# Kernel tuning notes

Measured on AMD Instinct MI355X. Metric: run time of the kernel, lower is better.

Reference implementation:

```python
import jax, jax.numpy as jnp
import numpy as np

H, W = 1280, 1920          # dense depth canvas (hardcoded in the torch module)
OUT_H, OUT_W = 427, 640    # kornia resize target
BIG = 1e9                  # sentinel coordinate for 'no seed yet'
FX = FY = 1000.0
CX, CY = 960.0, 640.0


def _jfa_nearest(valid):
    """1+JFA jump-flooding: (H,W) bool -> (H,W,2) float coords of nearest valid pixel.
    Replaces the faiss GpuIndexFlatL2 exact 1-NN over pixel coordinates."""
    rr, cc = jnp.meshgrid(jnp.arange(H, dtype=jnp.float32),
                          jnp.arange(W, dtype=jnp.float32), indexing='ij')
    coords = jnp.stack([rr, cc], axis=-1)                      # (H,W,2)
    nearest = jnp.where(valid[..., None], coords, BIG)
    best = jnp.sum((coords - nearest) ** 2, axis=-1)           # squared dist to current seed
    row_idx = jnp.arange(H)[:, None]
    col_idx = jnp.arange(W)[None, :]
    steps = [1, 1024, 512, 256, 128, 64, 32, 16, 8, 4, 2, 1]   # 1+JFA schedule, max dim 1920
    for k in steps:
        for dy in (-k, 0, k):
            for dx in (-k, 0, k):
                if dy == 0 and dx == 0:
                    continue
                cand = jnp.roll(nearest, (dy, dx), axis=(0, 1))
                src_r = row_idx - dy
                src_c = col_idx - dx
                ok = (src_r >= 0) & (src_r < H) & (src_c >= 0) & (src_c < W)
                cand = jnp.where(ok[..., None], cand, BIG)
                d = jnp.sum((coords - cand) ** 2, axis=-1)
                better = d < best
                best = jnp.where(better, d, best)
                nearest = jnp.where(better[..., None], cand, nearest)
    return nearest


def _one(points, pose, extrinsic, intrinsic):
    # projection path uses points.detach() in the torch code -> stop_gradient here
    p = jax.lax.stop_gradient(points)
    pts_world = p @ pose[:3, :3].T + pose[:3, 3]
    cam = pts_world @ extrinsic[:3, :3].T + extrinsic[:3, 3]
    proj = cam @ intrinsic.T
    u = proj[:, 0] / proj[:, 2]
    v = proj[:, 1] / proj[:, 2]
    r = jnp.floor(v).astype(jnp.int32)   # indices[..., [1,0]] swap -> row = v
    c = jnp.floor(u).astype(jnp.int32)
    depth_vals = jnp.linalg.norm(points, axis=-1)   # differentiable wrt points
    mask = (r >= 0) & (r < H) & (c >= 0) & (c < W)
    rs = jnp.where(mask, r, 0)
    cs = jnp.where(mask, c, 0)
    vals = jnp.where(mask, depth_vals, 0.0)
    # sparse scatter -> dense (duplicates sum, like torch.sparse to_dense)
    depth = jnp.zeros((H, W), jnp.float32).at[rs, cs].add(vals)
    valid = depth != 0
    nearest = jax.lax.stop_gradient(_jfa_nearest(valid))   # integer NN indices: non-diff
    nr = jnp.clip(nearest[..., 0], 0, H - 1).astype(jnp.int32)
    nc = jnp.clip(nearest[..., 1], 0, W - 1).astype(jnp.int32)
    rrf = jnp.arange(H, dtype=jnp.float32)[:, None]
    ccf = jnp.arange(W, dtype=jnp.float32)[None, :]
    dist = jnp.sqrt((rrf - nr.astype(jnp.float32)) ** 2 + (ccf - nc.astype(jnp.float32)) ** 2)
    dist = jnp.where(valid, 0.0, dist)          # dist_matrix only written at invalid pixels
    filled = jnp.where(valid, depth, depth[nr, nc])  # depth*(1-mask) + interpolated*mask
    out = jnp.stack([filled, dist], axis=0)     # (2, H, W)
    return jax.image.resize(out, (2, OUT_H, OUT_W), method='linear')


_batched = jax.jit(jax.vmap(_one))


def setup_inputs() -> dict:
    key = jax.random.key(0)
    B, N = 2, 120000
    ku, kv, kd = jax.random.split(key, 3)
    # sample pixels + depths, back-project so points land on the canvas
    u = jax.random.uniform(ku, (B, N), minval=0.0, maxval=W - 1.0)
    v = jax.random.uniform(kv, (B, N), minval=0.0, maxval=H - 1.0)
    d = jax.random.uniform(kd, (B, N), minval=2.0, maxval=50.0)
    x = (u - CX) * d / FX
    y = (v - CY) * d / FY
    points = jnp.stack([x, y, d], axis=-1).astype(jnp.float32)
    eye4 = jnp.broadcast_to(jnp.eye(4, dtype=jnp.float32), (B, 4, 4))
    K = jnp.array([[FX, 0.0, CX], [0.0, FY, CY], [0.0, 0.0, 1.0]], jnp.float32)
    intrinsic = jnp.broadcast_to(K, (B, 3, 3))
    return {"points": points, "pose": eye4, "extrinsic": eye4, "intrinsic": intrinsic}


def reference(points, pose, extrinsic, intrinsic):
    return _batched(points, pose, extrinsic, intrinsic)   # (B, 2, 427, 640)
```

## Files before the change

### kernel.cpp

```cpp
#include <hip/hip_runtime.h>
#include <math.h>
#include <limits.h>

#define HH 1280
#define WW 1920
#define OUT_H 427
#define OUT_W 640
#define SENT 0x7fff7fff

typedef short short2v __attribute__((ext_vector_type(2)));

__device__ __forceinline__ int dot22(int a, int P) {
#if __has_builtin(__builtin_amdgcn_sdot2)
    short2v s = __builtin_bit_cast(short2v, a) - __builtin_bit_cast(short2v, P);
    return __builtin_amdgcn_sdot2(s, s, 0, false);
#else
    int dr = (a >> 16) - (P >> 16);
    int dc = (short)a - (short)P;
    return dr * dr + dc * dc;
#endif
}
#define PICK(P, cur, dcur, cand)                    \
    {                                               \
        int _d = dot22((cand), (P));                \
        if (_d < (dcur)) { (cur) = (cand); (dcur) = _d; } \
    }

__global__ void scatter_k(const float* __restrict__ pts,
                          const float* __restrict__ pose,
                          const float* __restrict__ extr,
                          const float* __restrict__ intr,
                          float* __restrict__ depth, int N) {
    #pragma clang fp contract(off)
    int t = blockIdx.x * blockDim.x + threadIdx.x;
    int b = blockIdx.y;
    if (t >= N) return;
    const float* p = pts + ((long)b * N + t) * 3;
    float x = p[0], y = p[1], z = p[2];
    const float* P = pose + b * 16;
    const float* E = extr + b * 16;
    const float* K = intr + b * 9;
    float wx = ((x*P[0] + y*P[1]) + z*P[2]) + P[3];
    float wy = ((x*P[4] + y*P[5]) + z*P[6]) + P[7];
    float wz = ((x*P[8] + y*P[9]) + z*P[10]) + P[11];
    float cx = ((wx*E[0] + wy*E[1]) + wz*E[2]) + E[3];
    float cy = ((wx*E[4] + wy*E[5]) + wz*E[6]) + E[7];
    float cz = ((wx*E[8] + wy*E[9]) + wz*E[10]) + E[11];
    float px = (cx*K[0] + cy*K[1]) + cz*K[2];
    float py = (cx*K[3] + cy*K[4]) + cz*K[5];
    float pz = (cx*K[6] + cy*K[7]) + cz*K[8];
    float u = px / pz, v = py / pz;
    int r = (int)floorf(v), c = (int)floorf(u);
    if (r >= 0 && r < HH && c >= 0 && c < WW) {
        float dv = sqrtf((x*x + y*y) + z*z);
        atomicAdd(depth + ((long)b * HH + r) * WW + c, dv);
    }
}


template <bool FIRST>
__global__ __launch_bounds__(512)
void jfa12_k(const void* __restrict__ inv_, int* __restrict__ out, int k) {
    __shared__ int rows[4][WW];
    __shared__ int g1row[WW];
    int i = blockIdx.x, b = blockIdx.y;
    if (FIRST) {
        const float* dep = (const float*)inv_ + (long)b * HH * WW;
        #pragma unroll
        for (int t = 0; t < 4; ++t) {
            int r = i + t * k;
            if (r < HH) {
                const float4* src = reinterpret_cast<const float4*>(dep + (long)r * WW);
                for (int c4 = threadIdx.x; c4 < WW / 4; c4 += 512) {
                    float4 d = src[c4];
                    int4 v;
                    int c0 = c4 * 4, pb = r << 16;
                    v.x = (d.x != 0.0f) ? (pb | c0)       : SENT;
                    v.y = (d.y != 0.0f) ? (pb | (c0 + 1)) : SENT;
                    v.z = (d.z != 0.0f) ? (pb | (c0 + 2)) : SENT;
                    v.w = (d.w != 0.0f) ? (pb | (c0 + 3)) : SENT;
                    reinterpret_cast<int4*>(rows[t])[c4] = v;
                }
            } else {
                int4 sv; sv.x = sv.y = sv.z = sv.w = SENT;
                for (int c4 = threadIdx.x; c4 < WW / 4; c4 += 512)
                    reinterpret_cast<int4*>(rows[t])[c4] = sv;
            }
        }
    } else {
        const int* im = (const int*)inv_ + (long)b * HH * WW;
        #pragma unroll
        for (int t = 0; t < 4; ++t) {
            int r = i + t * k;
            if (r < HH) {
                const int4* src = reinterpret_cast<const int4*>(im + (long)r * WW);
                for (int c4 = threadIdx.x; c4 < WW / 4; c4 += 512)
                    reinterpret_cast<int4*>(rows[t])[c4] = src[c4];
            } else {
                int4 sv; sv.x = sv.y = sv.z = sv.w = SENT;
                for (int c4 = threadIdx.x; c4 < WW / 4; c4 += 512)
                    reinterpret_cast<int4*>(rows[t])[c4] = sv;
            }
        }
    }
    __syncthreads();
    bool rv1 = (i + k)     < HH;
    bool rv2 = (i + 2 * k) < HH;
    for (int j = threadIdx.x; j < WW; j += 512) {
        bool jk = (j + k < WW);
        int Pp = (i << 16) | j;
        int cur = rows[0][j];
        int dcur = dot22(cur, Pp);
        int c1 = jk ? rows[1][j + k] : SENT;
        PICK(Pp, cur, dcur, c1)
        int o1m = SENT;
        if (rv1) {
            int Pm = ((i + k) << 16) | j;
            int a = rows[1][j];
            int da = dot22(a, Pm);
            int c2 = jk ? rows[2][j + k] : SENT;
            PICK(Pm, a, da, c2)
            o1m = a;
        }
        PICK(Pp, cur, dcur, o1m)
        int o2q = SENT;
        int qj = j - k;
        if (rv1 && qj >= 0) {
            int Pq = ((i + k) << 16) | qj;
            int a0 = rows[1][qj];
            int d0 = dot22(a0, Pq);
            PICK(Pq, a0, d0, rows[2][j])
            int a1 = SENT;
            if (rv2) {
                int Pq2 = ((i + 2 * k) << 16) | qj;
                a1 = rows[2][qj];
                int d1 = dot22(a1, Pq2);
                PICK(Pq2, a1, d1, rows[3][j])
            }
            PICK(Pq, a0, d0, a1)
            o2q = a0;
        }
        PICK(Pp, cur, dcur, o2q)
        g1row[j] = cur;
    }
    __syncthreads();
    int* orow = out + ((long)b * HH + i) * WW;
    for (int j = threadIdx.x; j < WW; j += 512) {
        int Pp = (i << 16) | j;
        int a = g1row[j];
        int cur = a;
        int dcur = dot22(cur, Pp);
        int apk = (j + k < WW) ? g1row[j + k] : SENT;
        PICK(Pp, cur, dcur, apk)
        int o1m = SENT;
        int qj = j - k;
        if (qj >= 0) {
            int Pm = (i << 16) | qj;
            int am = g1row[qj];
            int dm = dot22(am, Pm);
            PICK(Pm, am, dm, a)
            o1m = am;
        }
        PICK(Pp, cur, dcur, o1m)
        orow[j] = cur;
    }
}

__global__ __launch_bounds__(512)
void jfa3r_k(const int* __restrict__ inv_, int* __restrict__ out, int dy, int k) {
    __shared__ int rows[4][WW];
    int i = blockIdx.x, b = blockIdx.y;
    const int* im = inv_ + (long)b * HH * WW;
    #pragma unroll
    for (int t = 0; t < 4; ++t) {
        int r = i - t * dy;
        if (r >= 0 && r < HH) {
            const int4* src = reinterpret_cast<const int4*>(im + (long)r * WW);
            for (int c4 = threadIdx.x; c4 < WW / 4; c4 += 512)
                reinterpret_cast<int4*>(rows[t])[c4] = src[c4];
        } else {
            int4 sv; sv.x = sv.y = sv.z = sv.w = SENT;
            for (int c4 = threadIdx.x; c4 < WW / 4; c4 += 512)
                reinterpret_cast<int4*>(rows[t])[c4] = sv;
        }
    }
    __syncthreads();
    bool rv1 = (unsigned)(i - dy)     < (unsigned)HH;
    bool rv2 = (unsigned)(i - 2 * dy) < (unsigned)HH;
    int* orow = out + ((long)b * HH + i) * WW;
    for (int j = threadIdx.x; j < WW; j += 512) {
        bool jk = (j + k < WW);
        int Pp = (i << 16) | j;
        int cur = rows[0][j];
        int dcur = dot22(cur, Pp);
        int c1 = jk ? rows[1][j + k] : SENT;
        PICK(Pp, cur, dcur, c1)
        int o1m = SENT;
        if (rv1) {
            int Pm = ((i - dy) << 16) | j;
            int a = rows[1][j];
            int da = dot22(a, Pm);
            int c2 = jk ? rows[2][j + k] : SENT;
            PICK(Pm, a, da, c2)
            o1m = a;
        }
        PICK(Pp, cur, dcur, o1m)
        int o2q = SENT;
        int qj = j - k;
        if (rv1 && qj >= 0) {
            int Pq = ((i - dy) << 16) | qj;
            int a0 = rows[1][qj];
            int d0 = dot22(a0, Pq);
            PICK(Pq, a0, d0, rows[2][j])
            int a1 = SENT;
            if (rv2) {
                int Pq2 = ((i - 2 * dy) << 16) | qj;
                a1 = rows[2][qj];
                int d1 = dot22(a1, Pq2);
                PICK(Pq2, a1, d1, rows[3][j])
            }
            PICK(Pq, a0, d0, a1)
            o2q = a0;
        }
        PICK(Pp, cur, dcur, o2q)
        orow[j] = cur;
    }
}

__global__ __launch_bounds__(256)
void hresize_k(const float* __restrict__ depth,
               const int* __restrict__ nr,
               float* __restrict__ tmp) {
    __shared__ float fbuf[WW];
    __shared__ float dbuf[WW];
    int i = blockIdx.x, b = blockIdx.y;
    const float* dep = depth + (long)b * HH * WW;
    const float* drow = dep + (long)i * WW;
    const int* nrow = nr + ((long)b * HH + i) * WW;
    for (int j = threadIdx.x; j < WW; j += 256) {
        float dv = drow[j];
        float f, dist;
        if (dv != 0.0f) { f = dv; dist = 0.0f; }
        else {
            int nn = nrow[j];
            int rr, cc;
            if (nn == SENT) { rr = HH - 1; cc = WW - 1; }
            else { rr = nn >> 16; cc = nn & 0xffff; }
            f = dep[(long)rr * WW + cc];
            float drr = (float)i - (float)rr, dcc = (float)j - (float)cc;
            dist = sqrtf(drr * drr + dcc * dcc);
        }
        fbuf[j] = f; dbuf[j] = dist;
    }
    __syncthreads();
    const float inv = 3.0f;
    for (int ow = threadIdx.x; ow < OUT_W; ow += 256) {
        float sf = (ow + 0.5f) * inv - 0.5f;
        int i0 = (int)ceilf(sf - inv);
        float a0 = 0.f, a1 = 0.f, wsum = 0.f;
        for (int k = 0; k < 7; ++k) {
            int iw = i0 + k;
            if (iw < 0 || iw >= WW) continue;
            float wgt = 1.0f - fabsf(sf - (float)iw) / inv;
            if (wgt <= 0.0f) continue;
            a0 += wgt * fbuf[iw]; a1 += wgt * dbuf[iw]; wsum += wgt;
        }
        long o = (((long)b * 2 + 0) * HH + i) * OUT_W + ow;
        tmp[o] = a0 / wsum;
        tmp[o + (long)HH * OUT_W] = a1 / wsum;
    }
}

__global__ void vresize_k(const float* __restrict__ tmp, float* __restrict__ out) {
    int ow = blockIdx.x * blockDim.x + threadIdx.x;
    int oh = blockIdx.y, bc = blockIdx.z;
    if (ow >= OUT_W) return;
    const float inv = (float)(1280.0 / 427.0);
    float sf = (oh + 0.5f) * inv - 0.5f;
    int i0 = (int)ceilf(sf - inv);
    float acc = 0.f, wsum = 0.f;
    const float* src = tmp + (long)bc * HH * OUT_W;
    for (int k = 0; k < 7; ++k) {
        int ih = i0 + k;
        if (ih < 0 || ih >= HH) continue;
        float wgt = 1.0f - fabsf(sf - (float)ih) / inv;
        if (wgt <= 0.0f) continue;
        acc += wgt * src[(long)ih * OUT_W + ow];
        wsum += wgt;
    }
    out[((long)bc * OUT_H + oh) * OUT_W + ow] = acc / wsum;
}

extern "C" void kernel_launch(void* const* d_in, const int* in_sizes, int n_in,
                              void* d_out, int out_size, void* d_ws, size_t ws_size,
                              hipStream_t stream) {
    const float* pts  = (const float*)d_in[0];
    const float* pose = (const float*)d_in[1];
    const float* extr = (const float*)d_in[2];
    const float* intr = (const float*)d_in[3];
    int B = in_sizes[1] / 16;
    int N = in_sizes[0] / (3 * B);

    char* ws = (char*)d_ws;
    size_t imgSz = (size_t)B * HH * WW;
    float* depth = (float*)ws;
    int*   nearA = (int*)(ws + imgSz * 4);
    int*   nearB = (int*)(ws + imgSz * 8);
    float* tmp   = (float*)(ws + imgSz * 12);

    hipMemsetAsync(depth, 0, imgSz * sizeof(float), stream);

    dim3 bs(256);
    scatter_k<<<dim3((N + 255) / 256, B), bs, 0, stream>>>(pts, pose, extr, intr, depth, N);

    dim3 gr(HH, B);
    int* cur = nearA; int* nxt = nearB;
    jfa12_k<true><<<gr, 512, 0, stream>>>(depth, cur, 1);
    jfa3r_k<<<gr, 512, 0, stream>>>(cur, nxt, +1, 1);
    { int* t2 = cur; cur = nxt; nxt = t2; }

    const int steps_rest[11] = {1024, 512, 256, 128, 64, 32, 16, 8, 4, 2, 1};
    for (int s = 0; s < 11; ++s) {
        int k = steps_rest[s];
        jfa12_k<false><<<gr, 512, 0, stream>>>(cur, nxt, k);
        { int* t2 = cur; cur = nxt; nxt = t2; }
        jfa3r_k<<<gr, 512, 0, stream>>>(cur, nxt, +k, k);
        { int* t2 = cur; cur = nxt; nxt = t2; }
    }

    hresize_k<<<dim3(HH, B), bs, 0, stream>>>(depth, cur, tmp);
    vresize_k<<<dim3((OUT_W + 255) / 256, OUT_H, B * 2), bs, 0, stream>>>(tmp, (float*)d_out);
}
```

Measured before the change: 497.4 us.

## Process row pairs (i, i+k) per block in JFA kernels to share loaded rows

Each JFA block now handles two output rows, i and i+k, drawn from a leader set, and loads 5 shared rows instead of 4 per single row. This reduces global row loads per output row from 4 to 2.5 and halves the block count. Stage-2 results are written back into the shared rows and kept in registers across unrolled column chunks. The cost is more shared memory per block (5 rows of 1920 ints), which may lower occupancy, plus extra index arithmetic.

```diff
diff --git a/kernel.cpp b/kernel.cpp
--- a/kernel.cpp
+++ b/kernel.cpp
@@ -25,6 +25,102 @@
         int _d = dot22((cand), (P));                \
         if (_d < (dcur)) { (cur) = (cand); (dcur) = _d; } \
     }
+
+__device__ __forceinline__ int g1_tree(int rows[][WW], int s, int r, int j, int k) {
+    bool rv1 = (r + k) < HH, rv2 = (r + 2 * k) < HH;
+    bool jk = (j + k < WW);
+    int Pp = (r << 16) | j;
+    int cur = rows[s][j];
+    int dcur = dot22(cur, Pp);
+    int c1 = jk ? rows[s + 1][j + k] : SENT;
+    PICK(Pp, cur, dcur, c1)
+    int o1m = SENT;
+    if (rv1) {
+        int Pm = ((r + k) << 16) | j;
+        int a = rows[s + 1][j];
+        int da = dot22(a, Pm);
+        int c2 = jk ? rows[s + 2][j + k] : SENT;
+        PICK(Pm, a, da, c2)
+        o1m = a;
+    }
+    PICK(Pp, cur, dcur, o1m)
+    int o2q = SENT;
+    int qj = j - k;
+    if (rv1 && qj >= 0) {
+        int Pq = ((r + k) << 16) | qj;
+        int a0 = rows[s + 1][qj];
+        int d0 = dot22(a0, Pq);
+        PICK(Pq, a0, d0, rows[s + 2][j])
+        int a1 = SENT;
+        if (rv2) {
+            int Pq2 = ((r + 2 * k) << 16) | qj;
+            a1 = rows[s + 2][qj];
+            int d1 = dot22(a1, Pq2);
+            PICK(Pq2, a1, d1, rows[s + 3][j])
+        }
+        PICK(Pq, a0, d0, a1)
+        o2q = a0;
+    }
+    PICK(Pp, cur, dcur, o2q)
+    return cur;
+}
+__device__ __forceinline__ int g2_tree(const int* g1row, int r, int j, int k) {
+    int Pp = (r << 16) | j;
+    int a = g1row[j];
+    int cur = a;
+    int dcur = dot22(cur, Pp);
+    int apk = (j + k < WW) ? g1row[j + k] : SENT;
+    PICK(Pp, cur, dcur, apk)
+    int o1m = SENT;
+    int qj = j - k;
+    if (qj >= 0) {
+        int Pm = (r << 16) | qj;
+        int am = g1row[qj];
+        int dm = dot22(am, Pm);
+        PICK(Pm, am, dm, a)
+        o1m = am;
+    }
+    PICK(Pp, cur, dcur, o1m)
+    return cur;
+}
+__device__ __forceinline__ int g3_tree(int rows[][WW], int s, int p, int j, int k) {
+    bool rv1 = (p - k) >= 0, rv2 = (p - 2 * k) >= 0;
+    bool jk = (j + k < WW);
+    int Pp = (p << 16) | j;
+    int cur = rows[s][j];
+    int dcur = dot22(cur, Pp);
+    int c1 = jk ? rows[s + 1][j + k] : SENT;
+    PICK(Pp, cur, dcur, c1)
+    int o1m = SENT;
+    if (rv1) {
+        int Pm = ((p - k) << 16) | j;
+        int a = rows[s + 1][j];
+        int da = dot22(a, Pm);
+        int c2 = jk ? rows[s + 2][j + k] : SENT;
+        PICK(Pm, a, da, c2)
+        o1m = a;
+    }
+    PICK(Pp, cur, dcur, o1m)
+    int o2q = SENT;
+    int qj = j - k;
+    if (rv1 && qj >= 0) {
+        int Pq = ((p - k) << 16) | qj;
+        int a0 = rows[s + 1][qj];
+        int d0 = dot22(a0, Pq);
+        PICK(Pq, a0, d0, rows[s + 2][j])
+        int a1 = SENT;
+        if (rv2) {
+            int Pq2 = ((p - 2 * k) << 16) | qj;
+            a1 = rows[s + 2][qj];
+            int d1 = dot22(a1, Pq2);
+            PICK(Pq2, a1, d1, rows[s + 3][j])
+        }
+        PICK(Pq, a0, d0, a1)
+        o2q = a0;
+    }
+    PICK(Pp, cur, dcur, o2q)
+    return cur;
+}
 
 __global__ void scatter_k(const float* __restrict__ pts,
                           const float* __restrict__ pose,
@@ -60,18 +156,21 @@
 
 template <bool FIRST>
 __global__ __launch_bounds__(512)
-void jfa12_k(const void* __restrict__ inv_, int* __restrict__ out, int k) {
-    __shared__ int rows[4][WW];
-    __shared__ int g1row[WW];
-    int i = blockIdx.x, b = blockIdx.y;
+void jfa12p_k(const void* __restrict__ inv_, int* __restrict__ out, int k) {
+    __shared__ int rows[5][WW];
+    int bx = blockIdx.x, b = blockIdx.y;
+    int i = (bx / k) * (2 * k) + (bx % k);
+    int ip = i + k;
+    bool hasP = ip < HH;
+    int tid = threadIdx.x;
     if (FIRST) {
         const float* dep = (const float*)inv_ + (long)b * HH * WW;
         #pragma unroll
-        for (int t = 0; t < 4; ++t) {
+        for (int t = 0; t < 5; ++t) {
             int r = i + t * k;
             if (r < HH) {
                 const float4* src = reinterpret_cast<const float4*>(dep + (long)r * WW);
-                for (int c4 = threadIdx.x; c4 < WW / 4; c4 += 512) {
+                for (int c4 = tid; c4 < WW / 4; c4 += 512) {
                     float4 d = src[c4];
                     int4 v;
                     int c0 = c4 * 4, pb = r << 16;
@@ -83,147 +182,88 @@
                 }
             } else {
                 int4 sv; sv.x = sv.y = sv.z = sv.w = SENT;
-                for (int c4 = threadIdx.x; c4 < WW / 4; c4 += 512)
+                for (int c4 = tid; c4 < WW / 4; c4 += 512)
                     reinterpret_cast<int4*>(rows[t])[c4] = sv;
             }
         }
     } else {
         const int* im = (const int*)inv_ + (long)b * HH * WW;
         #pragma unroll
-        for (int t = 0; t < 4; ++t) {
+        for (int t = 0; t < 5; ++t) {
             int r = i + t * k;
             if (r < HH) {
                 const int4* src = reinterpret_cast<const int4*>(im + (long)r * WW);
-                for (int c4 = threadIdx.x; c4 < WW / 4; c4 += 512)
+                for (int c4 = tid; c4 < WW / 4; c4 += 512)
                     reinterpret_cast<int4*>(rows[t])[c4] = src[c4];
             } else {
                 int4 sv; sv.x = sv.y = sv.z = sv.w = SENT;
-                for (int c4 = threadIdx.x; c4 < WW / 4; c4 += 512)
+                for (int c4 = tid; c4 < WW / 4; c4 += 512)
                     reinterpret_cast<int4*>(rows[t])[c4] = sv;
             }
         }
     }
     __syncthreads();
-    bool rv1 = (i + k)     < HH;
-    bool rv2 = (i + 2 * k) < HH;
-    for (int j = threadIdx.x; j < WW; j += 512) {
-        bool jk = (j + k < WW);
-        int Pp = (i << 16) | j;
-        int cur = rows[0][j];
-        int dcur = dot22(cur, Pp);
-        int c1 = jk ? rows[1][j + k] : SENT;
-        PICK(Pp, cur, dcur, c1)
-        int o1m = SENT;
-        if (rv1) {
-            int Pm = ((i + k) << 16) | j;
-            int a = rows[1][j];
-            int da = dot22(a, Pm);
-            int c2 = jk ? rows[2][j + k] : SENT;
-            PICK(Pm, a, da, c2)
-            o1m = a;
-        }
-        PICK(Pp, cur, dcur, o1m)
-        int o2q = SENT;
-        int qj = j - k;
-        if (rv1 && qj >= 0) {
-            int Pq = ((i + k) << 16) | qj;
-            int a0 = rows[1][qj];
-            int d0 = dot22(a0, Pq);
-            PICK(Pq, a0, d0, rows[2][j])
-            int a1 = SENT;
-            if (rv2) {
-                int Pq2 = ((i + 2 * k) << 16) | qj;
-                a1 = rows[2][qj];
-                int d1 = dot22(a1, Pq2);
-                PICK(Pq2, a1, d1, rows[3][j])
-            }
-            PICK(Pq, a0, d0, a1)
-            o2q = a0;
-        }
-        PICK(Pp, cur, dcur, o2q)
-        g1row[j] = cur;
-    }
-    __syncthreads();
-    int* orow = out + ((long)b * HH + i) * WW;
-    for (int j = threadIdx.x; j < WW; j += 512) {
-        int Pp = (i << 16) | j;
-        int a = g1row[j];
-        int cur = a;
-        int dcur = dot22(cur, Pp);
-        int apk = (j + k < WW) ? g1row[j + k] : SENT;
-        PICK(Pp, cur, dcur, apk)
-        int o1m = SENT;
-        int qj = j - k;
-        if (qj >= 0) {
-            int Pm = (i << 16) | qj;
-            int am = g1row[qj];
-            int dm = dot22(am, Pm);
-            PICK(Pm, am, dm, a)
-            o1m = am;
-        }
-        PICK(Pp, cur, dcur, o1m)
-        orow[j] = cur;
+    int g1a[4], g1b[4];
+    #pragma unroll
+    for (int u = 0; u < 4; ++u) {
+        int j = tid + u * 512;
+        if (j < WW) {
+            g1a[u] = g1_tree(rows, 0, i, j, k);
+            if (hasP) g1b[u] = g1_tree(rows, 1, ip, j, k);
+        }
+    }
+    __syncthreads();
+    #pragma unroll
+    for (int u = 0; u < 4; ++u) {
+        int j = tid + u * 512;
+        if (j < WW) {
+            rows[0][j] = g1a[u];
+            if (hasP) rows[1][j] = g1b[u];
+        }
+    }
+    __syncthreads();
+    int* obase = out + (long)b * HH * WW;
+    #pragma unroll
+    for (int u = 0; u < 4; ++u) {
+        int j = tid + u * 512;
+        if (j < WW) {
+            obase[(long)i * WW + j] = g2_tree(rows[0], i, j, k);
+            if (hasP) obase[(long)ip * WW + j] = g2_tree(rows[1], ip, j, k);
+        }
     }
 }
 
 __global__ __launch_bounds__(512)
-void jfa3r_k(const int* __restrict__ inv_, int* __restrict__ out, int dy, int k) {
-    __shared__ int rows[4][WW];
-    int i = blockIdx.x, b = blockIdx.y;
+void jfa3p_k(const int* __restrict__ inv_, int* __restrict__ out, int k) {
+    __shared__ int rows[5][WW];
+    int bx = blockIdx.x, b = blockIdx.y;
+    int i = (bx / k) * (2 * k) + (bx % k);
+    int ip = i + k;
+    bool hasP = ip < HH;
+    int tid = threadIdx.x;
     const int* im = inv_ + (long)b * HH * WW;
     #pragma unroll
-    for (int t = 0; t < 4; ++t) {
-        int r = i - t * dy;
+    for (int t = 0; t < 5; ++t) {
+        int r = ip - t * k;
         if (r >= 0 && r < HH) {
             const int4* src = reinterpret_cast<const int4*>(im + (long)r * WW);
-            for (int c4 = threadIdx.x; c4 < WW / 4; c4 += 512)
+            for (int c4 = tid; c4 < WW / 4; c4 += 512)
                 reinterpret_cast<int4*>(rows[t])[c4] = src[c4];
         } else {
             int4 sv; sv.x = sv.y = sv.z = sv.w = SENT;
-            for (int c4 = threadIdx.x; c4 < WW / 4; c4 += 512)
+            for (int c4 = tid; c4 < WW / 4; c4 += 512)
                 reinterpret_cast<int4*>(rows[t])[c4] = sv;
         }
     }
     __syncthreads();
-    bool rv1 = (unsigned)(i - dy)     < (unsigned)HH;
-    bool rv2 = (unsigned)(i - 2 * dy) < (unsigned)HH;
-    int* orow = out + ((long)b * HH + i) * WW;
-    for (int j = threadIdx.x; j < WW; j += 512) {
-        bool jk = (j + k < WW);
-        int Pp = (i << 16) | j;
-        int cur = rows[0][j];
-        int dcur = dot22(cur, Pp);
-        int c1 = jk ? rows[1][j + k] : SENT;
-        PICK(Pp, cur, dcur, c1)
-        int o1m = SENT;
-        if (rv1) {
-            int Pm = ((i - dy) << 16) | j;
-            int a = rows[1][j];
-            int da = dot22(a, Pm);
-            int c2 = jk ? rows[2][j + k] : SENT;
-            PICK(Pm, a, da, c2)
-            o1m = a;
-        }
-        PICK(Pp, cur, dcur, o1m)
-        int o2q = SENT;
-        int qj = j - k;
-        if (rv1 && qj >= 0) {
-            int Pq = ((i - dy) << 16) | qj;
-            int a0 = rows[1][qj];
-            int d0 = dot22(a0, Pq);
-            PICK(Pq, a0, d0, rows[2][j])
-            int a1 = SENT;
-            if (rv2) {
-                int Pq2 = ((i - 2 * dy) << 16) | qj;
-                a1 = rows[2][qj];
-                int d1 = dot22(a1, Pq2);
-                PICK(Pq2, a1, d1, rows[3][j])
-            }
-            PICK(Pq, a0, d0, a1)
-            o2q = a0;
-        }
-        PICK(Pp, cur, dcur, o2q)
-        orow[j] = cur;
+    int* obase = out + (long)b * HH * WW;
+    #pragma unroll
+    for (int u = 0; u < 4; ++u) {
+        int j = tid + u * 512;
+        if (j < WW) {
+            if (hasP) obase[(long)ip * WW + j] = g3_tree(rows, 0, ip, j, k);
+            obase[(long)i * WW + j] = g3_tree(rows, 1, i, j, k);
+        }
     }
 }
 
@@ -291,6 +331,16 @@
     out[((long)bc * OUT_H + oh) * OUT_W + ow] = acc / wsum;
 }
 
+static int nleaders(int k) {
+    int L = 0;
+    for (int m = 0;; ++m) {
+        int lo = 2 * m * k;
+        if (lo >= HH) break;
+        L += (HH - lo < k) ? (HH - lo) : k;
+    }
+    return L;
+}
+
 extern "C" void kernel_launch(void* const* d_in, const int* in_sizes, int n_in,
                               void* d_out, int out_size, void* d_ws, size_t ws_size,
                               hipStream_t stream) {
@@ -313,18 +363,20 @@
     dim3 bs(256);
     scatter_k<<<dim3((N + 255) / 256, B), bs, 0, stream>>>(pts, pose, extr, intr, depth, N);
 
-    dim3 gr(HH, B);
     int* cur = nearA; int* nxt = nearB;
-    jfa12_k<true><<<gr, 512, 0, stream>>>(depth, cur, 1);
-    jfa3r_k<<<gr, 512, 0, stream>>>(cur, nxt, +1, 1);
-    { int* t2 = cur; cur = nxt; nxt = t2; }
-
+    {
+        int L = nleaders(1);
+        jfa12p_k<true><<<dim3(L, B), 512, 0, stream>>>(depth, cur, 1);
+        jfa3p_k<<<dim3(L, B), 512, 0, stream>>>(cur, nxt, 1);
+        int* t2 = cur; cur = nxt; nxt = t2;
+    }
     const int steps_rest[11] = {1024, 512, 256, 128, 64, 32, 16, 8, 4, 2, 1};
     for (int s = 0; s < 11; ++s) {
         int k = steps_rest[s];
-        jfa12_k<false><<<gr, 512, 0, stream>>>(cur, nxt, k);
+        int L = nleaders(k);
+        jfa12p_k<false><<<dim3(L, B), 512, 0, stream>>>(cur, nxt, k);
         { int* t2 = cur; cur = nxt; nxt = t2; }
-        jfa3r_k<<<gr, 512, 0, stream>>>(cur, nxt, +k, k);
+        jfa3p_k<<<dim3(L, B), 512, 0, stream>>>(cur, nxt, k);
         { int* t2 = cur; cur = nxt; nxt = t2; }
     }
 
```

Result: no change. 503.5 us (+1.2%).
